# Optimization experiments

Hardware: AMD Instinct MI355X
Metric: run time of the kernel (lower is better)

Reference implementation:

```python
import jax, jax.numpy as jnp
import numpy as np


def setup_inputs() -> dict:
    key = jax.random.key(0)
    kx, kq, kk, kv = jax.random.split(key, 4)
    B, C, H, W = 8, 256, 48, 48
    scale = 1.0 / np.sqrt(C)
    return {
        "x": jax.random.normal(kx, (B, C, H, W), dtype=jnp.float32),
        "wq": jax.random.normal(kq, (C, C), dtype=jnp.float32) * scale,
        "wk": jax.random.normal(kk, (C, C), dtype=jnp.float32) * scale,
        "wv": jax.random.normal(kv, (C, C), dtype=jnp.float32) * scale,
    }


def reference(x, wq, wk, wv):
    # x: [B, C, H, W]; wq/wk/wv: [C_out, C_in] (squeezed 1x1 conv weights)
    B, C, H, W = x.shape
    xf = x.reshape(B, C, H * W)                       # [B, C, N]
    q = jnp.einsum('oc,bcn->bon', wq, xf)             # 1x1 conv == channel GEMM
    k = jnp.einsum('oc,bcn->bon', wk, xf)
    v = jnp.einsum('oc,bcn->bon', wv, xf)
    scores = jnp.einsum('bci,bcj->bij', q, k)         # [B, N, N] = q^T k
    weights = jax.nn.softmax(scores, axis=-1)
    attn = jnp.einsum('bij,bcj->bci', weights, v)     # value @ weights^T
    return x + attn.reshape(B, C, H, W)
```

## Files before the change

kernel.cpp:

```cpp
#include <hip/hip_runtime.h>
#include <hip/hip_bf16.h>


#define DEVI __device__ __forceinline__

typedef _Float16 f16x8 __attribute__((ext_vector_type(8)));
typedef float f32x4 __attribute__((ext_vector_type(4)));
typedef float f32x16 __attribute__((ext_vector_type(16)));

constexpr int Bn = 8, Cn = 256, Nn = 48 * 48;

#if defined(__has_builtin)
#if __has_builtin(__builtin_amdgcn_permlane32_swap)
#define HAVE_PL32 1
#endif
#endif

DEVI unsigned short f2h(float f) {
  _Float16 h = (_Float16)f;
  return __builtin_bit_cast(unsigned short, h);
}
DEVI float h2f(unsigned short u) {
  return (float)__builtin_bit_cast(_Float16, u);
}
DEVI unsigned pk2(float a, float b) {
  auto h = __builtin_amdgcn_cvt_pkrtz(a, b);
  return __builtin_bit_cast(unsigned, h);
}
DEVI void stage16(const unsigned short* g, unsigned short* l) {
  __builtin_amdgcn_global_load_lds(
      (const __attribute__((address_space(1))) void*)g,
      (__attribute__((address_space(3))) void*)l, 16, 0, 0);
}
DEVI void pl32swap(unsigned& a, unsigned& b) {
#ifdef HAVE_PL32
  auto r = __builtin_amdgcn_permlane32_swap(a, b, false, false);
  a = r[0];
  b = r[1];
#else
  unsigned sa = __shfl_xor(a, 32), sb = __shfl_xor(b, 32);
  bool hb = (threadIdx.x & 32) != 0;
  a = hb ? sb : a;
  b = hb ? b : sa;
#endif
}
DEVI void pl32swapf(float& a, float& b) {
  unsigned ua = __builtin_bit_cast(unsigned, a);
  unsigned ub = __builtin_bit_cast(unsigned, b);
  pl32swap(ua, ub);
  a = __builtin_bit_cast(float, ua);
  b = __builtin_bit_cast(float, ub);
}

#define MFMA16(a, b, c) __builtin_amdgcn_mfma_f32_16x16x32_f16((a), (b), (c), 0, 0, 0)
#define MFMA32(a, b, c) __builtin_amdgcn_mfma_f32_32x32x16_f16((a), (b), (c), 0, 0, 0)

__global__ __launch_bounds__(256) void cvt_w(const float* __restrict__ wq,
                                             const float* __restrict__ wk,
                                             const float* __restrict__ wv,
                                             unsigned short* __restrict__ o) {
  int idx = blockIdx.x * 256 + threadIdx.x;
  int mat = idx >> 16, off = idx & 65535;
  const float* s = (mat == 0) ? wq : (mat == 1) ? wk : wv;
  int ot = off >> 12, ks = (off >> 9) & 7, g = (off >> 7) & 3;
  int i = (off >> 3) & 15, j = off & 7;
  float v = s[(ot * 16 + i) * Cn + ks * 32 + g * 8 + j];
  if (mat == 0) v *= 1.44269504f;
  o[idx] = f2h(v);
}

__global__ __launch_bounds__(256) void qkv_proj(
    const float* __restrict__ x,
    const unsigned short* __restrict__ wqb, const unsigned short* __restrict__ wkb,
    const unsigned short* __restrict__ wvb,
    unsigned short* __restrict__ Qt, unsigned short* __restrict__ Ksw,
    unsigned short* __restrict__ Vsw) {
  __shared__ unsigned short xT[32][264];
  const int tid = threadIdx.x;
  const int n0 = blockIdx.x * 32;
  const int b = blockIdx.y;
  const float* xb = x + (size_t)b * Cn * Nn;
  {
    int c0 = tid >> 3;
    int nn = (tid & 7) * 4;
#pragma unroll
    for (int it = 0; it < 8; ++it) {
      int c = c0 + 32 * it;
      float4 v = *(const float4*)(xb + (size_t)c * Nn + n0 + nn);
      xT[nn + 0][c] = f2h(v.x);
      xT[nn + 1][c] = f2h(v.y);
      xT[nn + 2][c] = f2h(v.z);
      xT[nn + 3][c] = f2h(v.w);
    }
  }
  __syncthreads();
  const int lane = tid & 63, w = tid >> 6;
  const int i = lane & 15, g = lane >> 4;
  const int th = w & 1;
  const int wlo = g * 128 + i * 8;
  f16x8 xf[8];
#pragma unroll
  for (int ks = 0; ks < 8; ++ks)
    xf[ks] = *(const f16x8*)(&xT[th * 16 + i][32 * ks + 8 * g]);

  const int kb0 = n0 >> 5;
  if (w < 2) {
    const size_t tokbase = (size_t)b * Nn + n0 + th * 16;
    for (int ot = 0; ot < 16; ++ot) {
      f32x4 acc = {0.f, 0.f, 0.f, 0.f};
      const unsigned short* wr = wqb + ot * 4096 + wlo;
#pragma unroll
      for (int ks = 0; ks < 8; ++ks)
        acc = MFMA16(xf[ks], *(const f16x8*)(wr + 512 * ks), acc);
#pragma unroll
      for (int r = 0; r < 4; ++r)
        Qt[(tokbase + 4 * g + r) * Cn + ot * 16 + i] = f2h(acc[r]);
    }
  } else {
    unsigned short* kout = Ksw + (size_t)b * Nn * Cn + (size_t)kb0 * 8192
                         + ((i >> 3) & 1) * 256 + (i & 7);
    const int keyb = th * 16 + 4 * g;
    for (int ot = 0; ot < 16; ++ot) {
      f32x4 acc = {0.f, 0.f, 0.f, 0.f};
      const unsigned short* wr = wkb + ot * 4096 + wlo;
#pragma unroll
      for (int ks = 0; ks < 8; ++ks)
        acc = MFMA16(xf[ks], *(const f16x8*)(wr + 512 * ks), acc);
#pragma unroll
      for (int r = 0; r < 4; ++r)
        kout[ot * 512 + (keyb + r) * 8] = f2h(acc[r]);
    }
  }
  {
    unsigned short* vout = Vsw + (size_t)b * Nn * Cn + (size_t)kb0 * 8192
                         + th * 512 + ((i >> 3) & 1) * 256 + (i & 7);
    const int otb = (w >> 1) * 8;
    for (int oo = 0; oo < 8; ++oo) {
      const int ot = otb + oo;
      f32x4 acc = {0.f, 0.f, 0.f, 0.f};
      const unsigned short* wr = wvb + ot * 4096 + wlo;
#pragma unroll
      for (int ks = 0; ks < 8; ++ks)
        acc = MFMA16(*(const f16x8*)(wr + 512 * ks), xf[ks], acc);
#pragma unroll
      for (int r = 0; r < 4; ++r) {
        int c = ot * 16 + 4 * g + r;
        vout[(c >> 5) * 1024 + (c & 31) * 8] = f2h(acc[r]);
      }
    }
  }
}

__global__ __launch_bounds__(256, 2) void attn_split(
    const unsigned short* __restrict__ Qt, const unsigned short* __restrict__ Ksw,
    const unsigned short* __restrict__ Vsw,
    unsigned short* __restrict__ P, float* __restrict__ ml, int splits) {
  __shared__ unsigned short smem[24576];
  const int nblk = gridDim.x;
  const int cpx = nblk >> 3;
  const int swz = (blockIdx.x & 7) * cpx + (blockIdx.x >> 3);
  const int per_b = splits * 36;
  const int b = swz / per_b;
  const int rem = swz - b * per_b;
  const int s = rem / 36;
  const int qt = rem - s * 36;
  const int n0 = qt * 64;
  const int kn = Nn / splits;
  const int kb0 = (s * kn) >> 5;
  const int NT = kn / 32;

  const int tid = threadIdx.x, lane = tid & 63, w = tid >> 6;
  const int q = lane & 31, hi = lane >> 5;
  const int qtile = w & 1, chalf = w >> 1;
  const int q0 = n0 + qtile * 32;

  const unsigned short* Ksrc = Ksw + (size_t)b * Nn * Cn + tid * 8;
  const unsigned short* Vb = Vsw + (size_t)b * Nn * Cn + hi * 256 + q * 8
                           + (size_t)chalf * 4096;

  auto stageK = [&](int kbid, int buf) {
    unsigned short* dst = smem + buf * 8192 + w * 512;
    const unsigned short* src = Ksrc + (size_t)kbid * 8192;
#pragma unroll
    for (int c4 = 0; c4 < 4; ++c4)
      stage16(src + c4 * 2048, dst + c4 * 2048);
  };

  const int lo = hi * 512 + q * 16;

  const unsigned short* Qb = Qt + ((size_t)b * Nn + q0 + q) * Cn + 8 * hi;
  f16x8 qf[16];
#pragma unroll
  for (int ks = 0; ks < 16; ++ks) qf[ks] = *(const f16x8*)(Qb + 16 * ks);

  auto qkt = [&](int buf) -> f32x16 {
    const char* KsB = (const char*)smem + buf * 16384;
    f32x16 dd = (f32x16)(0.f);
#pragma unroll
    for (int ks = 0; ks < 16; ++ks)
      dd = MFMA32(*(const f16x8*)(KsB + ks * 1024 + lo), qf[ks], dd);
    return dd;
  };

  stageK(kb0, 0);
  stageK(kb0 + 1, 1);

  f32x16 acc[4];
#pragma unroll
  for (int ct = 0; ct < 4; ++ct) acc[ct] = (f32x16)(0.f);
  float m = -1e30f, lsum = 0.f;

  asm volatile("s_waitcnt vmcnt(4)" ::: "memory");
  __builtin_amdgcn_sched_barrier(0);
  __builtin_amdgcn_s_barrier();

  auto body = [&](int t, f32x16& dcur, f32x16& dnx) {
    const unsigned short* vp = Vb + (size_t)(kb0 + t) * 8192;
    f16x8 vf[8];
#pragma unroll
    for (int ct = 0; ct < 4; ++ct) {
      vf[2 * ct] = *(const f16x8*)(vp + ct * 1024);
      vf[2 * ct + 1] = *(const f16x8*)(vp + ct * 1024 + 512);
    }
    __builtin_amdgcn_sched_barrier(0);
    if (t + 2 < NT) stageK(kb0 + t + 2, (t + 2) % 3);

    if (t + 2 < NT)
      asm volatile("s_waitcnt vmcnt(12)" ::: "memory");
    else
      asm volatile("s_waitcnt vmcnt(8)" ::: "memory");
    __builtin_amdgcn_sched_barrier(0);
    __builtin_amdgcn_s_barrier();

    if (t + 1 < NT) dnx = qkt((t + 1) % 3);

    float u0 = fmaxf(dcur[0], dcur[1]),   u1 = fmaxf(dcur[2], dcur[3]);
    float u2 = fmaxf(dcur[4], dcur[5]),   u3 = fmaxf(dcur[6], dcur[7]);
    float u4 = fmaxf(dcur[8], dcur[9]),   u5 = fmaxf(dcur[10], dcur[11]);
    float u6 = fmaxf(dcur[12], dcur[13]), u7 = fmaxf(dcur[14], dcur[15]);
    float mx = fmaxf(fmaxf(fmaxf(u0, u1), fmaxf(u2, u3)),
                     fmaxf(fmaxf(u4, u5), fmaxf(u6, u7)));
    {
      float mc = mx;
      pl32swapf(mc, mx);
      mx = fmaxf(mc, mx);
    }
    if (__any(mx > m + 12.f)) {
      float mnew = fmaxf(m, mx);
      float alpha = __builtin_exp2f(m - mnew);
      m = mnew;
      lsum *= alpha;
#pragma unroll
      for (int ct = 0; ct < 4; ++ct)
#pragma unroll
        for (int r = 0; r < 16; ++r) acc[ct][r] *= alpha;
    }
    float p[16];
#pragma unroll
    for (int r = 0; r < 16; ++r) p[r] = __builtin_exp2f(dcur[r] - m);
    float cs = 0.f;
#pragma unroll
    for (int r = 0; r < 16; ++r) cs += p[r];
    lsum += cs;

    unsigned A0 = pk2(p[0], p[1]), A1 = pk2(p[2], p[3]);
    unsigned A2 = pk2(p[4], p[5]), A3 = pk2(p[6], p[7]);
    unsigned A4 = pk2(p[8], p[9]), A5 = pk2(p[10], p[11]);
    unsigned A6 = pk2(p[12], p[13]), A7 = pk2(p[14], p[15]);
    pl32swap(A0, A2);
    pl32swap(A1, A3);
    pl32swap(A4, A6);
    pl32swap(A5, A7);
    union { unsigned u[4]; f16x8 v; } pb0, pb1;
    pb0.u[0] = A0; pb0.u[1] = A1; pb0.u[2] = A2; pb0.u[3] = A3;
    pb1.u[0] = A4; pb1.u[1] = A5; pb1.u[2] = A6; pb1.u[3] = A7;

    __builtin_amdgcn_s_setprio(1);
    acc[0] = MFMA32(vf[0], pb0.v, acc[0]);
    acc[0] = MFMA32(vf[1], pb1.v, acc[0]);
    acc[1] = MFMA32(vf[2], pb0.v, acc[1]);
    acc[1] = MFMA32(vf[3], pb1.v, acc[1]);
    acc[2] = MFMA32(vf[4], pb0.v, acc[2]);
    acc[2] = MFMA32(vf[5], pb1.v, acc[2]);
    acc[3] = MFMA32(vf[6], pb0.v, acc[3]);
    acc[3] = MFMA32(vf[7], pb1.v, acc[3]);
    __builtin_amdgcn_s_setprio(0);
  };

  f32x16 dA = qkt(0), dB;
  for (int t = 0; t < NT; t += 2) {
    body(t, dA, dB);
    body(t + 1, dB, dA);
  }

  {
    float lc = lsum;
    pl32swapf(lc, lsum);
    lsum += lc;
  }
  const float rl = 1.f / lsum;
  unsigned short* Pb = P + (size_t)(s * Bn + b) * Cn * Nn;
#pragma unroll
  for (int ct = 0; ct < 4; ++ct)
#pragma unroll
    for (int r = 0; r < 16; ++r) {
      int c = 32 * (chalf * 4 + ct) + (r & 3) + 8 * (r >> 2) + 4 * hi;
      Pb[(size_t)c * Nn + q0 + q] = f2h(acc[ct][r] * rl);
    }
  if (!hi && !chalf)
    *(float2*)&ml[((size_t)(s * Bn + b) * Nn + q0 + q) * 2] = make_float2(m, lsum);
}

__global__ __launch_bounds__(256) void combine_k(
    const float* __restrict__ x, const unsigned short* __restrict__ P,
    const float* __restrict__ ml, float* __restrict__ out, int splits) {
  __shared__ float sc[4][32];
  const int tpb = Nn / 32;
  const int b = blockIdx.x / tpb;
  const int n0 = (blockIdx.x - b * tpb) * 32;
  const int t = threadIdx.x;
  if (t < 32) {
    const int n = n0 + t;
    const size_t sstr = (size_t)Bn * Nn * 2;
    const float* mlb = ml + ((size_t)b * Nn + n) * 2;
    float M = -1e30f;
    for (int s2 = 0; s2 < splits; ++s2) M = fmaxf(M, mlb[s2 * sstr]);
    float den = 0.f;
    for (int s2 = 0; s2 < splits; ++s2) {
      float g = __builtin_exp2f(mlb[s2 * sstr] - M) * mlb[s2 * sstr + 1];
      sc[s2][t] = g;
      den += g;
    }
    float rden = 1.f / den;
    for (int s2 = 0; s2 < splits; ++s2) sc[s2][t] *= rden;
  }
  __syncthreads();
  const int nl4 = (t & 7) * 4, c0 = t >> 3;
  const size_t pstr = (size_t)Bn * Cn * Nn;
  const float* xb = x + (size_t)b * Cn * Nn;
  float* ob = out + (size_t)b * Cn * Nn;
#pragma unroll
  for (int k = 0; k < 8; ++k) {
    const int c = c0 + 32 * k;
    const unsigned short* Pp = P + ((size_t)b * Cn + c) * Nn + n0 + nl4;
    f32x4 a = {0.f, 0.f, 0.f, 0.f};
    for (int s2 = 0; s2 < splits; ++s2) {
      ushort4 ph = *(const ushort4*)(Pp + s2 * pstr);
      f32x4 pv = {h2f(ph.x), h2f(ph.y), h2f(ph.z), h2f(ph.w)};
      f32x4 sw = {sc[s2][nl4 + 0], sc[s2][nl4 + 1], sc[s2][nl4 + 2], sc[s2][nl4 + 3]};
      a += sw * pv;
    }
    f32x4 xv = *(const f32x4*)(xb + (size_t)c * Nn + n0 + nl4);
    *(f32x4*)(ob + (size_t)c * Nn + n0 + nl4) = xv + a;
  }
}

extern "C" void kernel_launch(void* const* d_in, const int* in_sizes, int n_in,
                              void* d_out, int out_size, void* d_ws, size_t ws_size,
                              hipStream_t stream) {
  const float* x = (const float*)d_in[0];
  const float* wq = (const float*)d_in[1];
  const float* wk = (const float*)d_in[2];
  const float* wv = (const float*)d_in[3];
  float* out = (float*)d_out;

  unsigned short* wqb = (unsigned short*)d_ws;
  unsigned short* wkb = wqb + Cn * Cn;
  unsigned short* wvb = wkb + Cn * Cn;
  unsigned short* Qt = wvb + Cn * Cn;
  unsigned short* Ksw = Qt + (size_t)Bn * Nn * Cn;
  unsigned short* Vsw = Ksw + (size_t)Bn * Nn * Cn;
  unsigned short* P = Vsw + (size_t)Bn * Nn * Cn;

  const size_t baseB = (size_t)(3 * Cn * Cn + 3 * (size_t)Bn * Nn * Cn) * 2;
  const size_t perSplitB = (size_t)Bn * Nn * Cn * 2 + (size_t)Bn * Nn * 2 * 4;

  int splits = 1;
  if (baseB + 4 * perSplitB <= ws_size) splits = 4;
  else if (baseB + 2 * perSplitB <= ws_size) splits = 2;

  float* ml = (float*)(P + (size_t)splits * Bn * Nn * Cn);

  hipLaunchKernelGGL(cvt_w, dim3(3 * Cn * Cn / 256), dim3(256), 0, stream, wq, wk, wv, wqb);
  hipLaunchKernelGGL(qkv_proj, dim3(Nn / 32, Bn), dim3(256), 0, stream,
                     x, wqb, wkb, wvb, Qt, Ksw, Vsw);
  hipLaunchKernelGGL(attn_split, dim3(Bn * splits * 36), dim3(256), 0, stream,
                     Qt, Ksw, Vsw, P, ml, splits);
  hipLaunchKernelGGL(combine_k, dim3(Bn * Nn / 32), dim3(256), 0, stream,
                     x, P, ml, out, splits);
}
```

Measured before the change: 160.4 us.

## Stage QKV weight tiles through double-buffered LDS in projection kernel

The QKV projection kernel now copies each 16-row weight tile (Q/K pairs, then V pairs) into a double-buffered shared-memory buffer with stage16, prefetching the next tile while the current one feeds MFMAs. Previously every wave read its weights directly from global memory. The loop is restructured into 24 uniform steps with a block barrier each, so global loads are shared across waves and overlapped with compute. In exchange it adds 32KB of LDS and a barrier per step, which may reduce occupancy in a kernel that is likely a small share of total time.

After: 149.4 us. 1.07x faster.

```diff
diff --git a/kernel.cpp b/kernel.cpp
--- a/kernel.cpp
+++ b/kernel.cpp
@@ -76,6 +76,7 @@
     unsigned short* __restrict__ Qt, unsigned short* __restrict__ Ksw,
     unsigned short* __restrict__ Vsw) {
   __shared__ unsigned short xT[32][264];
+  __shared__ unsigned short wbuf[2][2][4096];
   const int tid = threadIdx.x;
   const int n0 = blockIdx.x * 32;
   const int b = blockIdx.y;
@@ -93,52 +94,67 @@
       xT[nn + 3][c] = f2h(v.w);
     }
   }
-  __syncthreads();
   const int lane = tid & 63, w = tid >> 6;
   const int i = lane & 15, g = lane >> 4;
   const int th = w & 1;
   const int wlo = g * 128 + i * 8;
+
+  auto stageW = [&](int e, int buf) {
+    const unsigned short* s0;
+    const unsigned short* s1;
+    if (e < 16) {
+      s0 = wqb + e * 4096;
+      s1 = wkb + e * 4096;
+    } else {
+      int ee = e - 16;
+      s0 = wvb + (2 * ee) * 4096;
+      s1 = wvb + (2 * ee + 1) * 4096;
+    }
+    stage16(s0 + w * 1024 + lane * 8,       &wbuf[buf][0][w * 1024]);
+    stage16(s0 + w * 1024 + 512 + lane * 8, &wbuf[buf][0][w * 1024 + 512]);
+    stage16(s1 + w * 1024 + lane * 8,       &wbuf[buf][1][w * 1024]);
+    stage16(s1 + w * 1024 + 512 + lane * 8, &wbuf[buf][1][w * 1024 + 512]);
+  };
+
+  stageW(0, 0);
+  __syncthreads();
+
   f16x8 xf[8];
 #pragma unroll
   for (int ks = 0; ks < 8; ++ks)
     xf[ks] = *(const f16x8*)(&xT[th * 16 + i][32 * ks + 8 * g]);
 
   const int kb0 = n0 >> 5;
-  if (w < 2) {
-    const size_t tokbase = (size_t)b * Nn + n0 + th * 16;
-    for (int ot = 0; ot < 16; ++ot) {
+  const size_t tokbase = (size_t)b * Nn + n0 + th * 16;
+  unsigned short* kout = Ksw + (size_t)b * Nn * Cn + (size_t)kb0 * 8192
+                       + ((i >> 3) & 1) * 256 + (i & 7);
+  const int keyb = th * 16 + 4 * g;
+  unsigned short* vout = Vsw + (size_t)b * Nn * Cn + (size_t)kb0 * 8192
+                       + th * 512 + ((i >> 3) & 1) * 256 + (i & 7);
+
+  for (int e = 0; e < 24; ++e) {
+    if (e) __syncthreads();
+    if (e + 1 < 24) stageW(e + 1, (e + 1) & 1);
+
+    const unsigned short* wr = &wbuf[e & 1][w >> 1][wlo];
+    if (e < 16) {
+      const int ot = e;
       f32x4 acc = {0.f, 0.f, 0.f, 0.f};
-      const unsigned short* wr = wqb + ot * 4096 + wlo;
 #pragma unroll
       for (int ks = 0; ks < 8; ++ks)
         acc = MFMA16(xf[ks], *(const f16x8*)(wr + 512 * ks), acc);
-#pragma unroll
-      for (int r = 0; r < 4; ++r)
-        Qt[(tokbase + 4 * g + r) * Cn + ot * 16 + i] = f2h(acc[r]);
-    }
-  } else {
-    unsigned short* kout = Ksw + (size_t)b * Nn * Cn + (size_t)kb0 * 8192
-                         + ((i >> 3) & 1) * 256 + (i & 7);
-    const int keyb = th * 16 + 4 * g;
-    for (int ot = 0; ot < 16; ++ot) {
+      if (w < 2) {
+#pragma unroll
+        for (int r = 0; r < 4; ++r)
+          Qt[(tokbase + 4 * g + r) * Cn + ot * 16 + i] = f2h(acc[r]);
+      } else {
+#pragma unroll
+        for (int r = 0; r < 4; ++r)
+          kout[ot * 512 + (keyb + r) * 8] = f2h(acc[r]);
+      }
+    } else {
+      const int ot = 2 * (e - 16) + (w >> 1);
       f32x4 acc = {0.f, 0.f, 0.f, 0.f};
-      const unsigned short* wr = wkb + ot * 4096 + wlo;
-#pragma unroll
-      for (int ks = 0; ks < 8; ++ks)
-        acc = MFMA16(xf[ks], *(const f16x8*)(wr + 512 * ks), acc);
-#pragma unroll
-      for (int r = 0; r < 4; ++r)
-        kout[ot * 512 + (keyb + r) * 8] = f2h(acc[r]);
-    }
-  }
-  {
-    unsigned short* vout = Vsw + (size_t)b * Nn * Cn + (size_t)kb0 * 8192
-                         + th * 512 + ((i >> 3) & 1) * 256 + (i & 7);
-    const int otb = (w >> 1) * 8;
-    for (int oo = 0; oo < 8; ++oo) {
-      const int ot = otb + oo;
-      f32x4 acc = {0.f, 0.f, 0.f, 0.f};
-      const unsigned short* wr = wvb + ot * 4096 + wlo;
 #pragma unroll
       for (int ks = 0; ks < 8; ++ks)
         acc = MFMA16(*(const f16x8*)(wr + 512 * ks), xf[ks], acc);
```
